# Performance work log

Hardware: AMD Instinct MI355X
Metric: run time of the kernel (lower is better)

## Reference

```python
import jax, jax.numpy as jnp
import numpy as np

N_NODES = 100000
N_EDGES = 1600000
N_GRAPHS = 64
IN_F = 128
H_F = 128
N_CLS = 10


def setup_inputs() -> dict:
    key = jax.random.key(0)
    ks = jax.random.split(key, 10)
    feat = jax.random.normal(ks[0], (N_NODES, IN_F), dtype=jnp.float32)
    W1 = jax.random.normal(ks[1], (IN_F, H_F), dtype=jnp.float32) * 0.05
    b1 = jax.random.normal(ks[2], (H_F,), dtype=jnp.float32) * 0.05
    W2 = jax.random.normal(ks[3], (H_F, H_F), dtype=jnp.float32) * 0.05
    b2 = jax.random.normal(ks[4], (H_F,), dtype=jnp.float32) * 0.05
    Wp = jax.random.normal(ks[5], (H_F, N_CLS), dtype=jnp.float32) * 0.05
    bp = jax.random.normal(ks[6], (N_CLS,), dtype=jnp.float32) * 0.05
    src = jax.random.randint(ks[7], (N_EDGES,), 0, N_NODES, dtype=jnp.int32)
    dst = jax.random.randint(ks[8], (N_EDGES,), 0, N_NODES, dtype=jnp.int32)
    graph_id = jnp.sort(jax.random.randint(ks[9], (N_NODES,), 0, N_GRAPHS, dtype=jnp.int32))
    return {"feat": feat, "W1": W1, "b1": b1, "W2": W2, "b2": b2,
            "Wp": Wp, "bp": bp, "src": src, "dst": dst, "graph_id": graph_id}


def reference(feat, W1, b1, W2, b2, Wp, bp, src, dst, graph_id):
    # copy_u + sum: each dst node sums features of its source neighbors
    def agg(h):
        return jax.ops.segment_sum(h[src], dst, num_segments=N_NODES)

    h = jax.nn.relu(agg(feat) @ W1 + b1)   # conv1 + ReLU
    h = jax.nn.relu(agg(h) @ W2 + b2)      # conv2 + ReLU (num_messagepasses=2)

    # dgl.mean_nodes: per-graph mean pooling over nodes
    sums = jax.ops.segment_sum(h, graph_id, num_segments=N_GRAPHS)      # [G, H]
    cnts = jax.ops.segment_sum(jnp.ones((N_NODES, 1), h.dtype), graph_id,
                               num_segments=N_GRAPHS)                    # [G, 1]
    graph_feats = sums / jnp.maximum(cnts, 1.0)
    return graph_feats @ Wp + bp
```

## Files before the change

kernel.cpp:

```cpp
#include <hip/hip_runtime.h>

#define NF 128
#define NGRAPHS 64
#define NCLS 10
#define NPARTS 256
#define PART_SHIFT 9
#define PART_NODES 512
#define PART_CAP 9216
#define SPLIT_TILE 4096
#define AS_STRIDE 136
#define SRC_BITS 17

typedef __attribute__((ext_vector_type(8))) short bf16x8;
typedef __attribute__((ext_vector_type(4))) float f32x4;
typedef __attribute__((ext_vector_type(8))) unsigned short u16x8;

__device__ __forceinline__ float bf2f(unsigned short u) {
    union { unsigned int i; float f; } v; v.i = ((unsigned int)u) << 16; return v.f;
}
__device__ __forceinline__ unsigned short f2bf(float f) {
    union { float f; unsigned int i; } v; v.f = f;
    unsigned int lsb = (v.i >> 16) & 1;
    v.i += 0x7fffu + lsb;
    return (unsigned short)(v.i >> 16);
}

__global__ __launch_bounds__(256) void prep_all(
    const float* __restrict__ feat, unsigned short* __restrict__ featbf,
    const float* __restrict__ W1, const float* __restrict__ W2,
    unsigned short* __restrict__ Wt1, unsigned short* __restrict__ Wt2,
    float* __restrict__ sums, int* __restrict__ gcur, int nv4) {
    int i = blockIdx.x * blockDim.x + threadIdx.x;
    if (i < nv4) {
        float4 v = ((const float4*)feat)[i];
        ushort4 o;
        o.x = f2bf(v.x); o.y = f2bf(v.y); o.z = f2bf(v.z); o.w = f2bf(v.w);
        ((ushort4*)featbf)[i] = o;
    }
    if (i < 2 * NF * NF) {
        const float* W = (i < NF * NF) ? W1 : W2;
        unsigned short* Wt = (i < NF * NF) ? Wt1 : Wt2;
        int id = i & (NF * NF - 1);
        int f = id >> 7;
        int k = id & 127;
        Wt[f * NF + k] = f2bf(W[k * NF + f]);
    }
    if (i < NGRAPHS * NF) sums[i] = 0.f;
    if (i < NPARTS) gcur[i] = 0;
}

__global__ __launch_bounds__(256) void split_kernel(
    const int* __restrict__ src, const int* __restrict__ dst,
    unsigned int* __restrict__ records, int* __restrict__ gcur, int ne) {
    __shared__ unsigned int stage[SPLIT_TILE];
    __shared__ int hcnt[NPARTS];
    __shared__ int hscan[NPARTS];
    __shared__ int hcur[NPARTS];
    __shared__ int hg[NPARTS];
    int t = threadIdx.x;
    int tile0 = blockIdx.x * SPLIT_TILE;
    int cnt = min(SPLIT_TILE, ne - tile0);
    if (cnt <= 0) return;
    hcnt[t] = 0;
    __syncthreads();
    for (int i = t; i < cnt; i += 256) {
        int d = dst[tile0 + i];
        atomicAdd(&hcnt[d >> PART_SHIFT], 1);
    }
    __syncthreads();
    hscan[t] = hcnt[t];
    __syncthreads();
    for (int off = 1; off < NPARTS; off <<= 1) {
        int v = (t >= off) ? hscan[t - off] : 0;
        __syncthreads();
        hscan[t] += v;
        __syncthreads();
    }
    hcur[t] = hscan[t] - hcnt[t];
    hg[t] = hcnt[t] ? atomicAdd(&gcur[t], hcnt[t]) : 0;
    __syncthreads();
    for (int i = t; i < cnt; i += 256) {
        int d = dst[tile0 + i];
        unsigned int s = (unsigned int)src[tile0 + i];
        int pos = atomicAdd(&hcur[d >> PART_SHIFT], 1);
        stage[pos] = (((unsigned int)(d & (PART_NODES - 1))) << SRC_BITS) | s;
    }
    __syncthreads();
    int grp = t >> 4;
    int lt = t & 15;
    for (int p = grp; p < NPARTS; p += 16) {
        int c = hcnt[p];
        if (c == 0) continue;
        int b = hscan[p] - c;
        int g = hg[p];
        if (g + c > PART_CAP) c = max(0, PART_CAP - g);
        unsigned int* outp = records + (size_t)p * PART_CAP + g;
        for (int i = lt; i < c; i += 16) outp[i] = stage[b + i];
    }
}

__global__ __launch_bounds__(256) void build_kernel(
    const unsigned int* __restrict__ records, const int* __restrict__ gcur,
    int* __restrict__ offs, int* __restrict__ eid, int n) {
    __shared__ int deg[PART_NODES];
    __shared__ int ps[NPARTS];
    __shared__ int wsum[4];
    int t = threadIdx.x;
    int p = blockIdx.x;

    ps[t] = min(gcur[t], PART_CAP);
    __syncthreads();
    for (int off = 1; off < NPARTS; off <<= 1) {
        int v = (t >= off) ? ps[t - off] : 0;
        __syncthreads();
        ps[t] += v;
        __syncthreads();
    }
    int L = min(gcur[p], PART_CAP);
    int base_g = ps[p] - L;
    if (p == 0 && t == 0) offs[n] = ps[NPARTS - 1];

    int lo = p << PART_SHIFT;
    int nn = min(n - lo, PART_NODES);
    if (nn <= 0) return;

    deg[t] = 0;
    deg[t + 256] = 0;
    __syncthreads();

    const unsigned int* rp = records + (size_t)p * PART_CAP;
    for (int i = t; i < L; i += 256) atomicAdd(&deg[rp[i] >> SRC_BITS], 1);
    __syncthreads();

    int v0 = deg[2 * t];
    int v1 = deg[2 * t + 1];
    int tsum = v0 + v1;
    int lane = t & 63, w = t >> 6;
    int sc = tsum;
    for (int off = 1; off < 64; off <<= 1) {
        int u = __shfl_up(sc, off, 64);
        if (lane >= off) sc += u;
    }
    if (lane == 63) wsum[w] = sc;
    __syncthreads();
    if (t == 0) {
        int a = 0;
        for (int k = 0; k < 4; ++k) { int v = wsum[k]; wsum[k] = a; a += v; }
    }
    __syncthreads();
    int run = sc - tsum + wsum[w];
    deg[2 * t] = run;
    if (2 * t < nn) offs[lo + 2 * t] = base_g + run;
    run += v0;
    deg[2 * t + 1] = run;
    if (2 * t + 1 < nn) offs[lo + 2 * t + 1] = base_g + run;
    __syncthreads();

    for (int i = t; i < L; i += 256) {
        unsigned int r = rp[i];
        int pos = atomicAdd(&deg[r >> SRC_BITS], 1);
        eid[base_g + pos] = (int)(r & ((1u << SRC_BITS) - 1));
    }
}

__global__ __launch_bounds__(256) void gather_gemm1(
    const unsigned short* __restrict__ x, const int* __restrict__ offs,
    const int* __restrict__ eid, const unsigned short* __restrict__ Wt,
    const float* __restrict__ bias, unsigned short* __restrict__ out, int n) {
    __shared__ unsigned short As[16 * AS_STRIDE];
    int wave = threadIdx.x >> 6;
    int lane = threadIdx.x & 63;
    int q = lane >> 4;
    int c = lane & 15;
    int node_base = blockIdx.x * 16;

    for (int i = 0; i < 4; ++i) {
        int row = wave * 4 + i;
        int node = node_base + row;
        float acc[8] = {0.f, 0.f, 0.f, 0.f, 0.f, 0.f, 0.f, 0.f};
        if (node < n) {
            int beg = offs[node];
            int end = offs[node + 1];
            int j = beg + q;
            for (; j + 4 < end; j += 8) {
                int s0 = eid[j];
                int s1 = eid[j + 4];
                u16x8 v0 = ((const u16x8*)(x + (size_t)s0 * NF))[c];
                u16x8 v1 = ((const u16x8*)(x + (size_t)s1 * NF))[c];
#pragma unroll
                for (int r = 0; r < 8; ++r) acc[r] += bf2f(v0[r]) + bf2f(v1[r]);
            }
            if (j < end) {
                int s0 = eid[j];
                u16x8 v0 = ((const u16x8*)(x + (size_t)s0 * NF))[c];
#pragma unroll
                for (int r = 0; r < 8; ++r) acc[r] += bf2f(v0[r]);
            }
        }
#pragma unroll
        for (int r = 0; r < 8; ++r) acc[r] += __shfl_xor(acc[r], 16, 64);
#pragma unroll
        for (int r = 0; r < 8; ++r) acc[r] += __shfl_xor(acc[r], 32, 64);
        if (q == 0) {
            u16x8 o;
#pragma unroll
            for (int r = 0; r < 8; ++r) o[r] = f2bf(acc[r]);
            *(u16x8*)(&As[row * AS_STRIDE + c * 8]) = o;
        }
    }
    __syncthreads();

    int m16 = c;
    int n0 = wave * 32;
    const unsigned short* b0r = Wt + (size_t)(n0 + m16) * NF + q * 8;
    const unsigned short* b1r = b0r + 16 * NF;
    f32x4 acc0 = {0.f, 0.f, 0.f, 0.f};
    f32x4 acc1 = {0.f, 0.f, 0.f, 0.f};
#pragma unroll
    for (int kk = 0; kk < 4; ++kk) {
        bf16x8 a  = *(const bf16x8*)(&As[m16 * AS_STRIDE + kk * 32 + q * 8]);
        bf16x8 b0 = *(const bf16x8*)(b0r + kk * 32);
        bf16x8 b1 = *(const bf16x8*)(b1r + kk * 32);
        acc0 = __builtin_amdgcn_mfma_f32_16x16x32_bf16(a, b0, acc0, 0, 0, 0);
        acc1 = __builtin_amdgcn_mfma_f32_16x16x32_bf16(a, b1, acc1, 0, 0, 0);
    }
    float bias0 = bias[n0 + m16];
    float bias1 = bias[n0 + 16 + m16];
#pragma unroll
    for (int r = 0; r < 4; ++r) {
        int node = node_base + q * 4 + r;
        if (node >= n) break;
        unsigned short* o = out + (size_t)node * NF;
        o[n0 + m16]      = f2bf(fmaxf(acc0[r] + bias0, 0.f));
        o[n0 + 16 + m16] = f2bf(fmaxf(acc1[r] + bias1, 0.f));
    }
}

__global__ __launch_bounds__(256) void gather_gemm2_pool(
    const unsigned short* __restrict__ x, const int* __restrict__ offs,
    const int* __restrict__ eid, const unsigned short* __restrict__ Wt,
    const float* __restrict__ bias, const int* __restrict__ gid,
    float* __restrict__ sums, int n) {
    __shared__ unsigned short As[16 * AS_STRIDE];
    __shared__ float hblk[16][NF];
    int wave = threadIdx.x >> 6;
    int lane = threadIdx.x & 63;
    int q = lane >> 4;
    int c = lane & 15;
    int node_base = blockIdx.x * 16;

    for (int i = 0; i < 4; ++i) {
        int row = wave * 4 + i;
        int node = node_base + row;
        float acc[8] = {0.f, 0.f, 0.f, 0.f, 0.f, 0.f, 0.f, 0.f};
        if (node < n) {
            int beg = offs[node];
            int end = offs[node + 1];
            int j = beg + q;
            for (; j + 4 < end; j += 8) {
                int s0 = eid[j];
                int s1 = eid[j + 4];
                u16x8 v0 = ((const u16x8*)(x + (size_t)s0 * NF))[c];
                u16x8 v1 = ((const u16x8*)(x + (size_t)s1 * NF))[c];
#pragma unroll
                for (int r = 0; r < 8; ++r) acc[r] += bf2f(v0[r]) + bf2f(v1[r]);
            }
            if (j < end) {
                int s0 = eid[j];
                u16x8 v0 = ((const u16x8*)(x + (size_t)s0 * NF))[c];
#pragma unroll
                for (int r = 0; r < 8; ++r) acc[r] += bf2f(v0[r]);
            }
        }
#pragma unroll
        for (int r = 0; r < 8; ++r) acc[r] += __shfl_xor(acc[r], 16, 64);
#pragma unroll
        for (int r = 0; r < 8; ++r) acc[r] += __shfl_xor(acc[r], 32, 64);
        if (q == 0) {
            u16x8 o;
#pragma unroll
            for (int r = 0; r < 8; ++r) o[r] = f2bf(acc[r]);
            *(u16x8*)(&As[row * AS_STRIDE + c * 8]) = o;
        }
    }
    __syncthreads();

    int m16 = c;
    int n0 = wave * 32;
    const unsigned short* b0r = Wt + (size_t)(n0 + m16) * NF + q * 8;
    const unsigned short* b1r = b0r + 16 * NF;
    f32x4 acc0 = {0.f, 0.f, 0.f, 0.f};
    f32x4 acc1 = {0.f, 0.f, 0.f, 0.f};
#pragma unroll
    for (int kk = 0; kk < 4; ++kk) {
        bf16x8 a  = *(const bf16x8*)(&As[m16 * AS_STRIDE + kk * 32 + q * 8]);
        bf16x8 b0 = *(const bf16x8*)(b0r + kk * 32);
        bf16x8 b1 = *(const bf16x8*)(b1r + kk * 32);
        acc0 = __builtin_amdgcn_mfma_f32_16x16x32_bf16(a, b0, acc0, 0, 0, 0);
        acc1 = __builtin_amdgcn_mfma_f32_16x16x32_bf16(a, b1, acc1, 0, 0, 0);
    }
    float bias0 = bias[n0 + m16];
    float bias1 = bias[n0 + 16 + m16];
#pragma unroll
    for (int r = 0; r < 4; ++r) {
        int row = q * 4 + r;
        hblk[row][n0 + m16]      = fmaxf(acc0[r] + bias0, 0.f);
        hblk[row][n0 + 16 + m16] = fmaxf(acc1[r] + bias1, 0.f);
    }
    __syncthreads();

    int t = threadIdx.x;
    if (t < NF) {
        float acc = 0.f;
        int cur = -1;
        int lim = min(16, n - node_base);
        for (int i = 0; i < lim; ++i) {
            int g = gid[node_base + i];
            if (g != cur) {
                if (cur >= 0) atomicAdd(&sums[cur * NF + t], acc);
                acc = 0.f;
                cur = g;
            }
            acc += bf2f(f2bf(hblk[i][t]));
        }
        if (cur >= 0) atomicAdd(&sums[cur * NF + t], acc);
    }
}

__device__ __forceinline__ int lower_bound_i(const int* a, int n, int key) {
    int lo = 0, hi = n;
    while (lo < hi) {
        int mid = (lo + hi) >> 1;
        if (a[mid] < key) lo = mid + 1; else hi = mid;
    }
    return lo;
}

__global__ __launch_bounds__(64) void final_kernel(
    const float* __restrict__ sums, const int* __restrict__ gid, int n,
    const float* __restrict__ Wp, const float* __restrict__ bp,
    float* __restrict__ out) {
    __shared__ int range[2];
    int g = blockIdx.x;
    int c = threadIdx.x;
    if (c == 0) range[0] = lower_bound_i(gid, n, g);
    if (c == 1) range[1] = lower_bound_i(gid, n, g + 1);
    __syncthreads();
    if (c >= NCLS) return;
    float cnt = fmaxf((float)(range[1] - range[0]), 1.0f);
    float inv = 1.0f / cnt;
    float acc = bp[c];
#pragma unroll 8
    for (int k = 0; k < NF; ++k) {
        acc += sums[g * NF + k] * inv * Wp[k * NCLS + c];
    }
    out[g * NCLS + c] = acc;
}

extern "C" void kernel_launch(void* const* d_in, const int* in_sizes, int n_in,
                              void* d_out, int out_size, void* d_ws, size_t ws_size,
                              hipStream_t stream) {
    const float* feat = (const float*)d_in[0];
    const float* W1   = (const float*)d_in[1];
    const float* b1   = (const float*)d_in[2];
    const float* W2   = (const float*)d_in[3];
    const float* b2   = (const float*)d_in[4];
    const float* Wp   = (const float*)d_in[5];
    const float* bp   = (const float*)d_in[6];
    const int*   src  = (const int*)d_in[7];
    const int*   dst  = (const int*)d_in[8];
    const int*   gid  = (const int*)d_in[9];

    int ne = in_sizes[7];
    int n  = in_sizes[9];

    unsigned short* featbf = (unsigned short*)d_ws;
    unsigned short* h1     = featbf + (size_t)n * NF;
    unsigned int* records = (unsigned int*)(h1 + (size_t)n * NF);
    int* eid      = (int*)(records + (size_t)NPARTS * PART_CAP);
    float* sums   = (float*)(eid + ne);
    int* gcur     = (int*)(sums + NGRAPHS * NF);
    unsigned short* Wt1 = (unsigned short*)(gcur + NPARTS);
    unsigned short* Wt2 = Wt1 + NF * NF;
    int* offs     = (int*)(Wt2 + NF * NF);

    int nv4 = n * NF / 4;
    int prepblocks = (nv4 + 255) / 256;
    int splitblocks = (ne + SPLIT_TILE - 1) / SPLIT_TILE;
    int buildblocks = (n + PART_NODES - 1) >> PART_SHIFT;
    int ggblocks = (n + 15) / 16;

    prep_all<<<prepblocks, 256, 0, stream>>>(feat, featbf, W1, W2, Wt1, Wt2,
                                             sums, gcur, nv4);
    split_kernel<<<splitblocks, 256, 0, stream>>>(src, dst, records, gcur, ne);
    build_kernel<<<buildblocks, 256, 0, stream>>>(records, gcur, offs, eid, n);

    gather_gemm1<<<ggblocks, 256, 0, stream>>>(featbf, offs, eid, Wt1, b1, h1, n);
    gather_gemm2_pool<<<ggblocks, 256, 0, stream>>>(h1, offs, eid, Wt2, b2, gid, sums, n);

    final_kernel<<<NGRAPHS, 64, 0, stream>>>(sums, gid, n, Wp, bp, (float*)d_out);
}
```

Baseline: 317.8 us.

## Fuse prep into split kernel and final projection into gemm2 via last-block ticket

Merges the feature/weight conversion into the edge split kernel with grid-stride loops and replaces zero-init of counters with a memset. The split kernel keeps src/dst in registers instead of reloading, and the build kernel caches partition records in LDS for its second pass. The final per-graph projection runs in the last block of gather_gemm2_pool using an atomic ticket, removing a separate launch. This reduces launch overhead and redundant global reads, but gives the conversion work fewer threads and adds a grid-wide fence.

```diff
diff --git a/kernel.cpp b/kernel.cpp
--- a/kernel.cpp
+++ b/kernel.cpp
@@ -25,19 +25,29 @@
     return (unsigned short)(v.i >> 16);
 }
 
-__global__ __launch_bounds__(256) void prep_all(
+__global__ __launch_bounds__(256) void split_prep_kernel(
+    const int* __restrict__ src, const int* __restrict__ dst,
+    unsigned int* __restrict__ records, int* __restrict__ gcur,
     const float* __restrict__ feat, unsigned short* __restrict__ featbf,
     const float* __restrict__ W1, const float* __restrict__ W2,
     unsigned short* __restrict__ Wt1, unsigned short* __restrict__ Wt2,
-    float* __restrict__ sums, int* __restrict__ gcur, int nv4) {
-    int i = blockIdx.x * blockDim.x + threadIdx.x;
-    if (i < nv4) {
+    float* __restrict__ sums, int ne, int nv4) {
+    __shared__ unsigned int stage[SPLIT_TILE];
+    __shared__ int hcnt[NPARTS];
+    __shared__ int hscan[NPARTS];
+    __shared__ int hcur[NPARTS];
+    __shared__ int hg[NPARTS];
+    int t = threadIdx.x;
+    int gtid = blockIdx.x * 256 + t;
+    int nthreads = gridDim.x * 256;
+
+    for (int i = gtid; i < nv4; i += nthreads) {
         float4 v = ((const float4*)feat)[i];
         ushort4 o;
         o.x = f2bf(v.x); o.y = f2bf(v.y); o.z = f2bf(v.z); o.w = f2bf(v.w);
         ((ushort4*)featbf)[i] = o;
     }
-    if (i < 2 * NF * NF) {
+    for (int i = gtid; i < 2 * NF * NF; i += nthreads) {
         const float* W = (i < NF * NF) ? W1 : W2;
         unsigned short* Wt = (i < NF * NF) ? Wt1 : Wt2;
         int id = i & (NF * NF - 1);
@@ -45,27 +55,22 @@
         int k = id & 127;
         Wt[f * NF + k] = f2bf(W[k * NF + f]);
     }
-    if (i < NGRAPHS * NF) sums[i] = 0.f;
-    if (i < NPARTS) gcur[i] = 0;
-}
-
-__global__ __launch_bounds__(256) void split_kernel(
-    const int* __restrict__ src, const int* __restrict__ dst,
-    unsigned int* __restrict__ records, int* __restrict__ gcur, int ne) {
-    __shared__ unsigned int stage[SPLIT_TILE];
-    __shared__ int hcnt[NPARTS];
-    __shared__ int hscan[NPARTS];
-    __shared__ int hcur[NPARTS];
-    __shared__ int hg[NPARTS];
-    int t = threadIdx.x;
+    for (int i = gtid; i < NGRAPHS * NF; i += nthreads) sums[i] = 0.f;
+
     int tile0 = blockIdx.x * SPLIT_TILE;
     int cnt = min(SPLIT_TILE, ne - tile0);
     if (cnt <= 0) return;
     hcnt[t] = 0;
     __syncthreads();
-    for (int i = t; i < cnt; i += 256) {
-        int d = dst[tile0 + i];
-        atomicAdd(&hcnt[d >> PART_SHIFT], 1);
+    int dv[16], sv[16];
+#pragma unroll
+    for (int k2 = 0; k2 < 16; ++k2) {
+        int i = k2 * 256 + t;
+        if (i < cnt) {
+            dv[k2] = dst[tile0 + i];
+            sv[k2] = src[tile0 + i];
+            atomicAdd(&hcnt[dv[k2] >> PART_SHIFT], 1);
+        }
     }
     __syncthreads();
     hscan[t] = hcnt[t];
@@ -79,11 +84,15 @@
     hcur[t] = hscan[t] - hcnt[t];
     hg[t] = hcnt[t] ? atomicAdd(&gcur[t], hcnt[t]) : 0;
     __syncthreads();
-    for (int i = t; i < cnt; i += 256) {
-        int d = dst[tile0 + i];
-        unsigned int s = (unsigned int)src[tile0 + i];
-        int pos = atomicAdd(&hcur[d >> PART_SHIFT], 1);
-        stage[pos] = (((unsigned int)(d & (PART_NODES - 1))) << SRC_BITS) | s;
+#pragma unroll
+    for (int k2 = 0; k2 < 16; ++k2) {
+        int i = k2 * 256 + t;
+        if (i < cnt) {
+            int d = dv[k2];
+            int pos = atomicAdd(&hcur[d >> PART_SHIFT], 1);
+            stage[pos] = (((unsigned int)(d & (PART_NODES - 1))) << SRC_BITS)
+                         | (unsigned int)sv[k2];
+        }
     }
     __syncthreads();
     int grp = t >> 4;
@@ -105,6 +114,7 @@
     __shared__ int deg[PART_NODES];
     __shared__ int ps[NPARTS];
     __shared__ int wsum[4];
+    __shared__ unsigned int rc[PART_CAP];
     int t = threadIdx.x;
     int p = blockIdx.x;
 
@@ -129,7 +139,11 @@
     __syncthreads();
 
     const unsigned int* rp = records + (size_t)p * PART_CAP;
-    for (int i = t; i < L; i += 256) atomicAdd(&deg[rp[i] >> SRC_BITS], 1);
+    for (int i = t; i < L; i += 256) {
+        unsigned int r = rp[i];
+        rc[i] = r;
+        atomicAdd(&deg[r >> SRC_BITS], 1);
+    }
     __syncthreads();
 
     int v0 = deg[2 * t];
@@ -157,7 +171,7 @@
     __syncthreads();
 
     for (int i = t; i < L; i += 256) {
-        unsigned int r = rp[i];
+        unsigned int r = rc[i];
         int pos = atomicAdd(&deg[r >> SRC_BITS], 1);
         eid[base_g + pos] = (int)(r & ((1u << SRC_BITS) - 1));
     }
@@ -236,13 +250,25 @@
     }
 }
 
+__device__ __forceinline__ int lower_bound_i(const int* a, int n, int key) {
+    int lo = 0, hi = n;
+    while (lo < hi) {
+        int mid = (lo + hi) >> 1;
+        if (a[mid] < key) lo = mid + 1; else hi = mid;
+    }
+    return lo;
+}
+
 __global__ __launch_bounds__(256) void gather_gemm2_pool(
     const unsigned short* __restrict__ x, const int* __restrict__ offs,
     const int* __restrict__ eid, const unsigned short* __restrict__ Wt,
     const float* __restrict__ bias, const int* __restrict__ gid,
-    float* __restrict__ sums, int n) {
+    float* __restrict__ sums, int* __restrict__ done,
+    const float* __restrict__ Wp, const float* __restrict__ bp,
+    float* __restrict__ out, int n) {
     __shared__ unsigned short As[16 * AS_STRIDE];
     __shared__ float hblk[16][NF];
+    __shared__ int ticket;
     int wave = threadIdx.x >> 6;
     int lane = threadIdx.x & 63;
     int q = lane >> 4;
@@ -325,36 +351,29 @@
         }
         if (cur >= 0) atomicAdd(&sums[cur * NF + t], acc);
     }
-}
-
-__device__ __forceinline__ int lower_bound_i(const int* a, int n, int key) {
-    int lo = 0, hi = n;
-    while (lo < hi) {
-        int mid = (lo + hi) >> 1;
-        if (a[mid] < key) lo = mid + 1; else hi = mid;
-    }
-    return lo;
-}
-
-__global__ __launch_bounds__(64) void final_kernel(
-    const float* __restrict__ sums, const int* __restrict__ gid, int n,
-    const float* __restrict__ Wp, const float* __restrict__ bp,
-    float* __restrict__ out) {
-    __shared__ int range[2];
-    int g = blockIdx.x;
-    int c = threadIdx.x;
-    if (c == 0) range[0] = lower_bound_i(gid, n, g);
-    if (c == 1) range[1] = lower_bound_i(gid, n, g + 1);
-    __syncthreads();
-    if (c >= NCLS) return;
-    float cnt = fmaxf((float)(range[1] - range[0]), 1.0f);
-    float inv = 1.0f / cnt;
-    float acc = bp[c];
-#pragma unroll 8
-    for (int k = 0; k < NF; ++k) {
-        acc += sums[g * NF + k] * inv * Wp[k * NCLS + c];
-    }
-    out[g * NCLS + c] = acc;
+
+    __threadfence();
+    __syncthreads();
+    if (t == 0) ticket = atomicAdd(done, 1);
+    __syncthreads();
+    if (ticket == (int)gridDim.x - 1) {
+        __threadfence();
+        if (t < NGRAPHS) {
+            int r0 = lower_bound_i(gid, n, t);
+            int r1 = lower_bound_i(gid, n, t + 1);
+            float inv = 1.0f / fmaxf((float)(r1 - r0), 1.0f);
+            float o[NCLS];
+#pragma unroll
+            for (int cc = 0; cc < NCLS; ++cc) o[cc] = bp[cc];
+            for (int k = 0; k < NF; ++k) {
+                float sv = sums[t * NF + k] * inv;
+#pragma unroll
+                for (int cc = 0; cc < NCLS; ++cc) o[cc] += sv * Wp[k * NCLS + cc];
+            }
+#pragma unroll
+            for (int cc = 0; cc < NCLS; ++cc) out[t * NCLS + cc] = o[cc];
+        }
+    }
 }
 
 extern "C" void kernel_launch(void* const* d_in, const int* in_sizes, int n_in,
@@ -380,23 +399,22 @@
     int* eid      = (int*)(records + (size_t)NPARTS * PART_CAP);
     float* sums   = (float*)(eid + ne);
     int* gcur     = (int*)(sums + NGRAPHS * NF);
-    unsigned short* Wt1 = (unsigned short*)(gcur + NPARTS);
+    int* done     = gcur + NPARTS;
+    unsigned short* Wt1 = (unsigned short*)(done + 1);
     unsigned short* Wt2 = Wt1 + NF * NF;
     int* offs     = (int*)(Wt2 + NF * NF);
 
     int nv4 = n * NF / 4;
-    int prepblocks = (nv4 + 255) / 256;
     int splitblocks = (ne + SPLIT_TILE - 1) / SPLIT_TILE;
     int buildblocks = (n + PART_NODES - 1) >> PART_SHIFT;
     int ggblocks = (n + 15) / 16;
 
-    prep_all<<<prepblocks, 256, 0, stream>>>(feat, featbf, W1, W2, Wt1, Wt2,
-                                             sums, gcur, nv4);
-    split_kernel<<<splitblocks, 256, 0, stream>>>(src, dst, records, gcur, ne);
+    hipMemsetAsync(gcur, 0, (NPARTS + 1) * sizeof(int), stream);
+    split_prep_kernel<<<splitblocks, 256, 0, stream>>>(
+        src, dst, records, gcur, feat, featbf, W1, W2, Wt1, Wt2, sums, ne, nv4);
     build_kernel<<<buildblocks, 256, 0, stream>>>(records, gcur, offs, eid, n);
 
     gather_gemm1<<<ggblocks, 256, 0, stream>>>(featbf, offs, eid, Wt1, b1, h1, n);
-    gather_gemm2_pool<<<ggblocks, 256, 0, stream>>>(h1, offs, eid, Wt2, b2, gid, sums, n);
-
-    final_kernel<<<NGRAPHS, 64, 0, stream>>>(sums, gid, n, Wp, bp, (float*)d_out);
-}
+    gather_gemm2_pool<<<ggblocks, 256, 0, stream>>>(
+        h1, offs, eid, Wt2, b2, gid, sums, done, Wp, bp, (float*)d_out, n);
+}
```

Measured after the change: 897.4 us. 2.82x slower.
